# Kernel optimization log

Measured on AMD Instinct MI355X. Metric: run time of the kernel, lower is better.

Reference implementation:

```python
import jax, jax.numpy as jnp
import numpy as np

L = 8192   # residues / nodes
E = 524288 # contact-map edges (avg degree 64)
NEG_SLOPE = 0.2  # PyG GATConv default negative_slope


def gat_layer(x, src, dst, Wg, asrc, adst, bias):
    """PyG-style GATConv (v1), concat heads, eval mode (no dropout).
    x: [L, F_in]; Wg: [F_in, H*C]; asrc/adst: [H, C]; bias: [H*C]."""
    H, C = asrc.shape
    h = (x @ Wg).reshape(L, H, C)                      # [L,H,C]
    a_s = jnp.einsum('nhc,hc->nh', h, asrc)            # [L,H]
    a_d = jnp.einsum('nhc,hc->nh', h, adst)            # [L,H]
    e = jax.nn.leaky_relu(a_s[src] + a_d[dst], NEG_SLOPE)  # [E',H]
    # softmax over incoming edges of each destination node
    m = jax.ops.segment_max(e, dst, num_segments=L)
    ex = jnp.exp(e - m[dst])
    denom = jax.ops.segment_sum(ex, dst, num_segments=L)
    alpha = ex / (denom[dst] + 1e-16)                  # [E',H]
    msg = h[src] * alpha[:, :, None]                   # [E',H,C]
    out = jax.ops.segment_sum(msg, dst, num_segments=L)  # [L,H,C]
    return out.reshape(L, H * C) + bias


def setup_inputs() -> dict:
    key = jax.random.key(0)
    ks = jax.random.split(key, 16)
    def g(k, shape, scale=0.05):
        return (jax.random.normal(k, shape, dtype=jnp.float32) * scale)
    return {
        'input_seq': jax.random.normal(ks[0], (1, L, 26), dtype=jnp.float32),
        'edge_index': jax.random.randint(ks[1], (2, E), 0, L, dtype=jnp.int32),
        'W1': g(ks[2], (26, 1024)),
        'W2': g(ks[3], (1024, 256)),
        'Wg1': g(ks[4], (256, 256)),
        'asrc1': g(ks[5], (4, 64)),
        'adst1': g(ks[6], (4, 64)),
        'b1': g(ks[7], (256,)),
        'Wg2': g(ks[8], (256, 512)),
        'asrc2': g(ks[9], (4, 128)),
        'adst2': g(ks[10], (4, 128)),
        'b2': g(ks[11], (512,)),
        'fcW': g(ks[12], (512, 512)),
        'fcb': g(ks[13], (512,)),
        'outW': g(ks[14], (512, 489)),
        'outb': g(ks[15], (489,)),
    }


def reference(input_seq, edge_index, W1, W2, Wg1, asrc1, adst1, b1,
              Wg2, asrc2, adst2, b2, fcW, fcb, outW, outb):
    # input_layer: Linear(26,1024,no bias) -> ReLU -> Linear(1024,256,no bias)
    x = jax.nn.relu(input_seq[0] @ W1) @ W2            # [L,256]
    # add self-loops (PyG GATConv default)
    loops = jnp.arange(L, dtype=edge_index.dtype)
    src = jnp.concatenate([edge_index[0], loops])
    dst = jnp.concatenate([edge_index[1], loops])
    # two GAT layers with ReLU activation
    x = jax.nn.relu(gat_layer(x, src, dst, Wg1, asrc1, adst1, b1))  # [L,256]
    x = jax.nn.relu(gat_layer(x, src, dst, Wg2, asrc2, adst2, b2))  # [L,512]
    # sum-pool over residues (x.sum(dim=1) with batch=1)
    pooled = x.sum(axis=0, keepdims=True)              # [1,512]
    # fc layers (dropout inactive in eval)
    h = jax.nn.relu(pooled @ fcW + fcb)                # [1,512]
    return h @ outW + outb                             # [1,489]
```

## Files before the change

### kernel.cpp

```cpp
#include <hip/hip_runtime.h>
#include <hip/hip_bf16.h>

constexpr int L = 8192;
constexpr int H = 4;

typedef __attribute__((ext_vector_type(8))) short bf16x8;
typedef __attribute__((ext_vector_type(8))) unsigned short u16x8;
typedef __attribute__((ext_vector_type(4))) float f32x4;

static __device__ __forceinline__ float lrelu(float e) {
  return e > 0.f ? e : 0.2f * e;
}
static __device__ __forceinline__ float b2f(unsigned short s) {
  return __uint_as_float(((unsigned)s) << 16);
}
static __device__ __forceinline__ unsigned short f2b(float f) {
  __hip_bfloat16 h = __float2bfloat16(f);
  return *reinterpret_cast<unsigned short*>(&h);
}

__global__ __launch_bounds__(256) void conv_combo(
    const float* __restrict__ seq, const float* __restrict__ W1,
    const float* __restrict__ W2, const float* __restrict__ Wg1,
    const float* __restrict__ Wg2, const float* __restrict__ fcW,
    const float* __restrict__ outW, const int* __restrict__ ei,
    const float* __restrict__ as1, const float* __restrict__ ad1,
    const float* __restrict__ as2, const float* __restrict__ ad2,
    int E, int Etot,
    __hip_bfloat16* __restrict__ xb, __hip_bfloat16* __restrict__ W1t,
    __hip_bfloat16* __restrict__ W2t, __hip_bfloat16* __restrict__ Wg1t,
    __hip_bfloat16* __restrict__ Wg2t, float* __restrict__ fcWt,
    float* __restrict__ outWt, float* __restrict__ wa2,
    int* __restrict__ deg, int* __restrict__ rank) {
  __shared__ float tile[32][33];
  if (blockIdx.x < 992) {
    int b = blockIdx.x;
    const float* src; void* dst; bool obf16; int K, N, Kout, kt, nt;
    if (b < 256)               { src = W2;  dst = W2t;  obf16 = true;  K = 1024; N = 256; Kout = 1024; nt = b & 7;  kt = b >> 3; }
    else if ((b -= 256) < 64)  { src = Wg1; dst = Wg1t; obf16 = true;  K = 256;  N = 256; Kout = 256;  nt = b & 7;  kt = b >> 3; }
    else if ((b -= 64) < 128)  { src = Wg2; dst = Wg2t; obf16 = true;  K = 256;  N = 512; Kout = 256;  nt = b & 15; kt = b >> 4; }
    else if ((b -= 128) < 256) { src = fcW; dst = fcWt; obf16 = false; K = 512;  N = 512; Kout = 512;  nt = b & 15; kt = b >> 4; }
    else if ((b -= 256) < 256) { src = outW;dst = outWt;obf16 = false; K = 512;  N = 489; Kout = 512;  nt = b & 15; kt = b >> 4; }
    else { b -= 256;             src = W1;  dst = W1t;  obf16 = true;  K = 26;   N = 1024;Kout = 32;   nt = b;      kt = 0; }
    int t = threadIdx.x;
    int lr = t >> 3, lc4 = (t & 7) * 4;
    int gk = kt * 32 + lr, gn = nt * 32 + lc4;
    float4 v = {0.f, 0.f, 0.f, 0.f};
    if (gk < K) {
      const float* p = &src[(size_t)gk * N + gn];
      v.x = (gn + 0 < N) ? p[0] : 0.f;
      v.y = (gn + 1 < N) ? p[1] : 0.f;
      v.z = (gn + 2 < N) ? p[2] : 0.f;
      v.w = (gn + 3 < N) ? p[3] : 0.f;
    }
    tile[lr][lc4 + 0] = v.x; tile[lr][lc4 + 1] = v.y;
    tile[lr][lc4 + 2] = v.z; tile[lr][lc4 + 3] = v.w;
    __syncthreads();
    int on = nt * 32 + lr, ok = kt * 32 + lc4;
    if (on >= N || ok >= Kout) return;
    float o0 = tile[lc4 + 0][lr], o1 = tile[lc4 + 1][lr];
    float o2 = tile[lc4 + 2][lr], o3 = tile[lc4 + 3][lr];
    if (obf16) {
      ushort4 u = {f2b(o0), f2b(o1), f2b(o2), f2b(o3)};
      *(ushort4*)&((__hip_bfloat16*)dst)[(size_t)on * Kout + ok] = u;
    } else {
      float4 u = {o0, o1, o2, o3};
      *(float4*)&((float*)dst)[(size_t)on * Kout + ok] = u;
    }
    return;
  }
  int i = (blockIdx.x - 992) * 256 + threadIdx.x;
  if (i < 262144) { int r = i >> 5, k = i & 31;
    xb[i] = __float2bfloat16(k < 26 ? seq[r * 26 + k] : 0.f); return; }
  i -= 262144;
  if (i < 2048) {
    int k = i >> 3, o = i & 7, h = o & 3;
    const float* av = (o < 4) ? as1 : ad1;
    float s = 0.f;
    for (int c = 0; c < 64; c++) s += Wg1[k * 256 + h * 64 + c] * av[h * 64 + c];
    Wg1t[(size_t)(256 + o) * 256 + k] = __float2bfloat16(s); return; }
  i -= 2048;
  if (i < 2048) {
    int k = i >> 3, o = i & 7, h = o & 3;
    const float* av = (o < 4) ? as2 : ad2;
    float s = 0.f;
    for (int c = 0; c < 128; c++) s += Wg2[k * 512 + h * 128 + c] * av[h * 128 + c];
    wa2[i] = s; return; }
  i -= 2048;
  if (i < 14336) {
    ((__hip_bfloat16*)Wg1t)[(size_t)264 * 256 + i] = __float2bfloat16(0.f); return; }
  i -= 14336;
  if (i < Etot) {
    int dst = (i < E) ? ei[E + i] : (i - E);
    rank[i] = atomicAdd(&deg[dst], 1);
  }
}

template<int BK, bool RELU, bool ASD>
__global__ __launch_bounds__(256) void gemm_big(
    const __hip_bfloat16* __restrict__ A, const __hip_bfloat16* __restrict__ Bt,
    __hip_bfloat16* __restrict__ C, float* __restrict__ asd,
    int M, int N, int K) {
  __shared__ __align__(16) short As[128][BK + 8];
  __shared__ __align__(16) short Bs[64][BK + 8];
  int tid = threadIdx.x;
  int m0 = blockIdx.y * 128, n0 = blockIdx.x * 64;
  int w = tid >> 6, lane = tid & 63;
  int wm = (w >> 1) * 64, wn = (w & 1) * 32;
  f32x4 acc[4][2] = {};
  for (int k0 = 0; k0 < K; k0 += BK) {
    if constexpr (BK == 64) {
#pragma unroll
      for (int i = 0; i < 4; i++) {
        int ch = i * 256 + tid; int r = ch >> 3, kg = ch & 7;
        *(bf16x8*)&As[r][kg * 8] = *(const bf16x8*)&A[(size_t)(m0 + r) * K + k0 + kg * 8];
      }
#pragma unroll
      for (int i = 0; i < 2; i++) {
        int ch = i * 256 + tid; int r = ch >> 3, kg = ch & 7;
        *(bf16x8*)&Bs[r][kg * 8] = *(const bf16x8*)&Bt[(size_t)(n0 + r) * K + k0 + kg * 8];
      }
    } else {
#pragma unroll
      for (int i = 0; i < 2; i++) {
        int ch = i * 256 + tid; int r = ch >> 2, kg = ch & 3;
        *(bf16x8*)&As[r][kg * 8] = *(const bf16x8*)&A[(size_t)(m0 + r) * K + k0 + kg * 8];
      }
      { int r = tid >> 2, kg = tid & 3;
        *(bf16x8*)&Bs[r][kg * 8] = *(const bf16x8*)&Bt[(size_t)(n0 + r) * K + k0 + kg * 8]; }
    }
    __syncthreads();
    int kk = (lane >> 4) * 8;
#pragma unroll
    for (int ks = 0; ks < BK / 32; ks++) {
      bf16x8 af[4], bfr[2];
#pragma unroll
      for (int m = 0; m < 4; m++)
        af[m] = *(const bf16x8*)&As[wm + m * 16 + (lane & 15)][ks * 32 + kk];
#pragma unroll
      for (int n = 0; n < 2; n++)
        bfr[n] = *(const bf16x8*)&Bs[wn + n * 16 + (lane & 15)][ks * 32 + kk];
#pragma unroll
      for (int m = 0; m < 4; m++)
#pragma unroll
        for (int n = 0; n < 2; n++)
          acc[m][n] = __builtin_amdgcn_mfma_f32_16x16x32_bf16(af[m], bfr[n], acc[m][n], 0, 0, 0);
    }
    __syncthreads();
  }
#pragma unroll
  for (int m = 0; m < 4; m++) {
#pragma unroll
    for (int n = 0; n < 2; n++) {
      int col = n0 + wn + n * 16 + (lane & 15);
#pragma unroll
      for (int j = 0; j < 4; j++) {
        int row = m0 + wm + m * 16 + (lane >> 4) * 4 + j;
        float v = acc[m][n][j];
        if (RELU) v = fmaxf(v, 0.f);
        if (!ASD) {
          C[(size_t)row * N + col] = __float2bfloat16(v);
        } else {
          if (col < N) C[(size_t)row * N + col] = __float2bfloat16(v);
          else if (col < N + 8) asd[(size_t)row * 8 + (col - N)] = v;
        }
      }
    }
  }
}

__global__ __launch_bounds__(1024) void scan_deg(const int* __restrict__ deg,
                                                 int* __restrict__ row_start,
                                                 float* __restrict__ pooled) {
  __shared__ int wsum[16];
  int t = threadIdx.x;
  if (t < 512) pooled[t] = 0.f;
  int lane = t & 63, w = t >> 6;
  int local[8];
  int sum = 0;
#pragma unroll
  for (int j = 0; j < 8; j++) { local[j] = deg[t * 8 + j]; sum += local[j]; }
  int v = sum;
#pragma unroll
  for (int off = 1; off < 64; off <<= 1) {
    int u = __shfl_up(v, off);
    if (lane >= off) v += u;
  }
  if (lane == 63) wsum[w] = v;
  __syncthreads();
  int woff = 0;
  for (int i = 0; i < w; i++) woff += wsum[i];
  int base = woff + v - sum;
#pragma unroll
  for (int j = 0; j < 8; j++) { row_start[t * 8 + j] = base; base += local[j]; }
  if (t == 1023) row_start[L] = base;
}

__global__ void scatter_edges(const int* __restrict__ ei, int E, int Etot,
                              const int* __restrict__ row_start,
                              const int* __restrict__ rank, int* __restrict__ csr_src) {
  int e = blockIdx.x * blockDim.x + threadIdx.x;
  if (e >= Etot) return;
  int srcv, dstv;
  if (e < E) { srcv = ei[e]; dstv = ei[E + e]; } else { srcv = dstv = e - E; }
  csr_src[row_start[dstv] + rank[e]] = srcv;
}

template<int C, int PHASES, bool ASD2>
__global__ __launch_bounds__(128) void gat_fused(
    const __hip_bfloat16* __restrict__ hfeat, const float* __restrict__ a_sd,
    const int* __restrict__ row_start, const int* __restrict__ csr_src,
    const float* __restrict__ bias, __hip_bfloat16* __restrict__ out,
    const float* __restrict__ wa2, float* __restrict__ a_sd2) {
  constexpr int HC = 4 * C;
  constexpr int CP = HC / PHASES;
  constexpr int BATCH = 16;
  static_assert(CP == 256, "phase width must be 256");
  int wid = threadIdx.x >> 6, lane = threadIdx.x & 63;
  int n = blockIdx.x * 2 + wid;
  int c0 = blockIdx.y * CP + lane * 4;
  int hh = c0 / C;
  int rs = row_start[n], re = row_start[n + 1];
  float4 ad4 = *(const float4*)&a_sd[(size_t)n * 8 + 4];
  float bv[4];
#pragma unroll
  for (int k = 0; k < 4; k++) bv[k] = bias[c0 + k];

  __shared__ float s_w[2][64][4];
  float dp[4] = {0.f, 0.f, 0.f, 0.f};
  float acc[4] = {0.f, 0.f, 0.f, 0.f};
  const unsigned short* hbase = (const unsigned short*)hfeat;

  int base = rs;
  int cnt = min(64, re - rs);
  int srcv = 0;
  float4 as4 = {0.f, 0.f, 0.f, 0.f};
  if (lane < cnt) {
    srcv = csr_src[rs + lane];
    as4 = *(const float4*)&a_sd[(size_t)srcv * 8];
  }

  while (base < re) {
    float w0 = 0.f, w1 = 0.f, w2 = 0.f, w3 = 0.f;
    if (lane < cnt) {
      w0 = __expf(lrelu(as4.x + ad4.x));
      w1 = __expf(lrelu(as4.y + ad4.y));
      w2 = __expf(lrelu(as4.z + ad4.z));
      w3 = __expf(lrelu(as4.w + ad4.w));
    }
    dp[0] += w0; dp[1] += w1; dp[2] += w2; dp[3] += w3;
    float4 wv = {w0, w1, w2, w3};
    *(float4*)&s_w[wid][lane][0] = wv;
    asm volatile("s_waitcnt lgkmcnt(0)" ::: "memory");
    int cur_src = srcv;
    int cur_cnt = cnt;
    int nbase = base + 64;
    bool have_next = nbase < re;
    cnt = min(64, re - nbase);
    srcv = 0;
    if (have_next && lane < cnt) srcv = csr_src[nbase + lane];
    float4 nas4 = {0.f, 0.f, 0.f, 0.f};
    bool did_asd = false;

    int j = 0;
    for (; j + BATCH <= cur_cnt; j += BATCH) {
      int srs[BATCH];
#pragma unroll
      for (int k = 0; k < BATCH; k++) srs[k] = __builtin_amdgcn_readlane(cur_src, j + k);
      ushort4 v[BATCH];
#pragma unroll
      for (int k = 0; k < BATCH; k++)
        v[k] = *(const ushort4*)&hbase[(size_t)srs[k] * HC + c0];
      if (j == BATCH && have_next) {
        if (lane < cnt) nas4 = *(const float4*)&a_sd[(size_t)srcv * 8];
        did_asd = true;
      }
#pragma unroll
      for (int k = 0; k < BATCH; k++) {
        float av = s_w[wid][j + k][hh];
        acc[0] = fmaf(av, b2f(v[k].x), acc[0]);
        acc[1] = fmaf(av, b2f(v[k].y), acc[1]);
        acc[2] = fmaf(av, b2f(v[k].z), acc[2]);
        acc[3] = fmaf(av, b2f(v[k].w), acc[3]);
      }
    }
    if (have_next && !did_asd && lane < cnt)
      nas4 = *(const float4*)&a_sd[(size_t)srcv * 8];
    for (; j < cur_cnt; j++) {
      int sr = __builtin_amdgcn_readlane(cur_src, j);
      float av = s_w[wid][j][hh];
      ushort4 v = *(const ushort4*)&hbase[(size_t)sr * HC + c0];
      acc[0] = fmaf(av, b2f(v.x), acc[0]);
      acc[1] = fmaf(av, b2f(v.y), acc[1]);
      acc[2] = fmaf(av, b2f(v.z), acc[2]);
      acc[3] = fmaf(av, b2f(v.w), acc[3]);
    }
    as4 = nas4;
    base = nbase;
  }

#pragma unroll
  for (int off = 32; off > 0; off >>= 1) {
#pragma unroll
    for (int h = 0; h < 4; h++) dp[h] += __shfl_xor(dp[h], off);
  }
  float dsel = hh == 0 ? dp[0] : hh == 1 ? dp[1] : hh == 2 ? dp[2] : dp[3];
  float inv = 1.f / (dsel + 1e-16f);

#pragma unroll
  for (int k = 0; k < 4; k++)
    acc[k] = fmaxf(fmaf(acc[k], inv, bv[k]), 0.f);
  ushort4 ov = {f2b(acc[0]), f2b(acc[1]), f2b(acc[2]), f2b(acc[3])};
  *(ushort4*)((unsigned short*)out + (size_t)n * HC + c0) = ov;

  if constexpr (ASD2) {
    float p[8] = {};
#pragma unroll
    for (int q = 0; q < 4; q++) {
      const float* wr = &wa2[(size_t)(c0 + q) * 8];
#pragma unroll
      for (int o = 0; o < 8; o++) p[o] = fmaf(acc[q], wr[o], p[o]);
    }
#pragma unroll
    for (int off = 32; off > 0; off >>= 1) {
#pragma unroll
      for (int o = 0; o < 8; o++) p[o] += __shfl_xor(p[o], off);
    }
    if (lane == 0) {
      float4 p0 = {p[0], p[1], p[2], p[3]};
      float4 p1 = {p[4], p[5], p[6], p[7]};
      *(float4*)&a_sd2[(size_t)n * 8 + 0] = p0;
      *(float4*)&a_sd2[(size_t)n * 8 + 4] = p1;
    }
  }
}

__global__ __launch_bounds__(512) void col_sum_bf16(const __hip_bfloat16* __restrict__ x,
                                                    float* __restrict__ pooled) {
  int t = threadIdx.x;
  float acc = 0.f;
  for (int r = blockIdx.x; r < L; r += 64)
    acc += b2f(*(const unsigned short*)&x[(size_t)r * 512 + t]);
  atomicAdd(&pooled[t], acc);
}

__global__ __launch_bounds__(256) void fc1(const float* __restrict__ pooled,
                                           const float* __restrict__ Wt,
                                           const float* __restrict__ b,
                                           float* __restrict__ out) {
  __shared__ float pv[512];
  __shared__ float red[256];
  int t = threadIdx.x;
  pv[t] = pooled[t]; pv[t + 256] = pooled[t + 256];
  __syncthreads();
  int ol = t >> 4;
  int o = blockIdx.x * 16 + ol;
  int ks = (t & 15) * 32;
  float p = 0.f;
  const float* wr = &Wt[(size_t)o * 512 + ks];
#pragma unroll
  for (int kk = 0; kk < 32; kk++) p = fmaf(pv[ks + kk], wr[kk], p);
  red[t] = p;
  __syncthreads();
  if ((t & 15) == 0) {
    float s2 = 0.f;
#pragma unroll
    for (int i = 0; i < 16; i++) s2 += red[ol * 16 + i];
    out[o] = fmaxf(s2 + b[o], 0.f);
  }
}

__global__ __launch_bounds__(256) void fc2(const float* __restrict__ h,
                                           const float* __restrict__ Wt,
                                           const float* __restrict__ outb,
                                           float* __restrict__ out) {
  __shared__ float pv[512];
  __shared__ float red[256];
  int t = threadIdx.x;
  pv[t] = h[t]; pv[t + 256] = h[t + 256];
  __syncthreads();
  int ol = t >> 4;
  int o = blockIdx.x * 16 + ol;
  int ks = (t & 15) * 32;
  float p = 0.f;
  const float* wr = &Wt[(size_t)o * 512 + ks];
#pragma unroll
  for (int kk = 0; kk < 32; kk++) p = fmaf(pv[ks + kk], wr[kk], p);
  red[t] = p;
  __syncthreads();
  if ((t & 15) == 0 && o < 489) {
    float s2 = 0.f;
#pragma unroll
    for (int i = 0; i < 16; i++) s2 += red[ol * 16 + i];
    out[o] = s2 + outb[o];
  }
}

extern "C" void kernel_launch(void* const* d_in, const int* in_sizes, int n_in,
                              void* d_out, int out_size, void* d_ws, size_t ws_size,
                              hipStream_t stream) {
  const float* seq   = (const float*)d_in[0];
  const int*   ei    = (const int*)d_in[1];
  const float* W1    = (const float*)d_in[2];
  const float* W2    = (const float*)d_in[3];
  const float* Wg1   = (const float*)d_in[4];
  const float* asrc1 = (const float*)d_in[5];
  const float* adst1 = (const float*)d_in[6];
  const float* b1    = (const float*)d_in[7];
  const float* Wg2   = (const float*)d_in[8];
  const float* asrc2 = (const float*)d_in[9];
  const float* adst2 = (const float*)d_in[10];
  const float* b2    = (const float*)d_in[11];
  const float* fcW   = (const float*)d_in[12];
  const float* fcb   = (const float*)d_in[13];
  const float* outW  = (const float*)d_in[14];
  const float* outb  = (const float*)d_in[15];
  float* outp = (float*)d_out;

  const int E = in_sizes[1] / 2;
  const int Etot = E + L;

  char* ws = (char*)d_ws;
  __hip_bfloat16* mlp1 = (__hip_bfloat16*)(ws + 0);
  __hip_bfloat16* out2 = (__hip_bfloat16*)(ws + 0);
  __hip_bfloat16* h2   = (__hip_bfloat16*)(ws + (16u << 20));
  __hip_bfloat16* x0   = (__hip_bfloat16*)(ws + (24u << 20));
  __hip_bfloat16* h1   = (__hip_bfloat16*)(ws + (28u << 20));
  __hip_bfloat16* out1 = (__hip_bfloat16*)(ws + (32u << 20));
  size_t off = (36u << 20);
  __hip_bfloat16* xb   = (__hip_bfloat16*)(ws + off); off += (size_t)L * 32 * 2;
  __hip_bfloat16* W1t  = (__hip_bfloat16*)(ws + off); off += (size_t)1024 * 32 * 2;
  __hip_bfloat16* W2t  = (__hip_bfloat16*)(ws + off); off += (size_t)256 * 1024 * 2;
  __hip_bfloat16* Wg1t = (__hip_bfloat16*)(ws + off); off += (size_t)320 * 256 * 2;
  __hip_bfloat16* Wg2t = (__hip_bfloat16*)(ws + off); off += (size_t)512 * 256 * 2;
  float* fcWt  = (float*)(ws + off); off += (size_t)512 * 512 * 4;
  float* outWt = (float*)(ws + off); off += (size_t)512 * 512 * 4;
  int* csr_src = (int*)(ws + off); off += (size_t)Etot * 4;
  int* rank    = (int*)(ws + off); off += (size_t)Etot * 4;
  off = (off + 255) & ~(size_t)255;
  int* row_start = (int*)(ws + off); off += (size_t)(L + 1) * 4;
  off = (off + 255) & ~(size_t)255;
  int* deg    = (int*)(ws + off); off += (size_t)L * 4;
  float* a_sd1 = (float*)(ws + off); off += (size_t)L * 8 * 4;
  float* a_sd2 = (float*)(ws + off); off += (size_t)L * 8 * 4;
  float* wa2 = (float*)(ws + off); off += 2048 * 4;
  float* pooled = (float*)(ws + off); off += 512 * 4;
  float* hbuf   = (float*)(ws + off); off += 512 * 4;

  hipMemsetAsync(deg, 0, (size_t)L * 4, stream);

  int convN = 262144 + 2048 + 2048 + 14336 + Etot;
  int convB = (convN + 255) / 256;
  conv_combo<<<992 + convB, 256, 0, stream>>>(
      seq, W1, W2, Wg1, Wg2, fcW, outW, ei, asrc1, adst1, asrc2, adst2, E, Etot,
      xb, W1t, W2t, Wg1t, Wg2t, fcWt, outWt, wa2, deg, rank);

  scan_deg<<<1, 1024, 0, stream>>>(deg, row_start, pooled);
  scatter_edges<<<(Etot + 255) / 256, 256, 0, stream>>>(ei, E, Etot, row_start, rank, csr_src);

  gemm_big<32, true, false><<<dim3(16, 64), 256, 0, stream>>>(xb, W1t, mlp1, nullptr, L, 1024, 32);
  gemm_big<64, false, false><<<dim3(4, 64), 256, 0, stream>>>(mlp1, W2t, x0, nullptr, L, 256, 1024);

  gemm_big<64, false, true><<<dim3(5, 64), 256, 0, stream>>>(x0, Wg1t, h1, a_sd1, L, 256, 256);
  gat_fused<64, 1, true><<<dim3(4096, 1), 128, 0, stream>>>(h1, a_sd1, row_start, csr_src, b1, out1, wa2, a_sd2);

  gemm_big<64, false, false><<<dim3(8, 64), 256, 0, stream>>>(out1, Wg2t, h2, nullptr, L, 512, 256);
  gat_fused<128, 2, false><<<dim3(4096, 2), 128, 0, stream>>>(h2, a_sd2, row_start, csr_src, b2, out2, nullptr, nullptr);

  col_sum_bf16<<<64, 512, 0, stream>>>(out2, pooled);
  fc1<<<32, 256, 0, stream>>>(pooled, fcWt, fcb, hbuf);
  fc2<<<31, 256, 0, stream>>>(hbuf, outWt, outb, outp);
}
```

Baseline: 221.7 us.

## Precompute GAT attention weights and softmax denominators in a separate kernel

Adds a calc_alpha kernel that computes the per-edge exp(leaky_relu) attention weights once, stores them as bf16 along with per-node inverse denominators, and then has gat_fused read these instead of recomputing them. The aim is to stop the second GAT layer's two column-phase blocks from each redoing the exp, gather and reduction work, and to drop the dependent a_sd gather from the aggregation loop. In exchange it adds two kernel launches, an extra read/write pass over edge-sized alpha data, and rounds the unnormalised weights to bf16, which loses some precision.

```diff
diff --git a/kernel.cpp b/kernel.cpp
--- a/kernel.cpp
+++ b/kernel.cpp
@@ -206,9 +206,42 @@
   csr_src[row_start[dstv] + rank[e]] = srcv;
 }
 
+__global__ __launch_bounds__(256) void calc_alpha(
+    const float* __restrict__ a_sd, const int* __restrict__ row_start,
+    const int* __restrict__ csr_src, unsigned short* __restrict__ alpha,
+    float* __restrict__ inv4) {
+  int wid = threadIdx.x >> 6, lane = threadIdx.x & 63;
+  int n = blockIdx.x * 4 + wid;
+  int rs = row_start[n], re = row_start[n + 1];
+  float4 ad4 = *(const float4*)&a_sd[(size_t)n * 8 + 4];
+  float dp[4] = {0.f, 0.f, 0.f, 0.f};
+  for (int base = rs + lane; base < re; base += 64) {
+    int src = csr_src[base];
+    float4 as4 = *(const float4*)&a_sd[(size_t)src * 8];
+    float w0 = __expf(lrelu(as4.x + ad4.x));
+    float w1 = __expf(lrelu(as4.y + ad4.y));
+    float w2 = __expf(lrelu(as4.z + ad4.z));
+    float w3 = __expf(lrelu(as4.w + ad4.w));
+    dp[0] += w0; dp[1] += w1; dp[2] += w2; dp[3] += w3;
+    ushort4 wv = {f2b(w0), f2b(w1), f2b(w2), f2b(w3)};
+    *(ushort4*)&alpha[(size_t)base * 4] = wv;
+  }
+#pragma unroll
+  for (int off = 32; off > 0; off >>= 1) {
+#pragma unroll
+    for (int h = 0; h < 4; h++) dp[h] += __shfl_xor(dp[h], off);
+  }
+  if (lane == 0) {
+    float4 iv = {1.f / (dp[0] + 1e-16f), 1.f / (dp[1] + 1e-16f),
+                 1.f / (dp[2] + 1e-16f), 1.f / (dp[3] + 1e-16f)};
+    *(float4*)&inv4[(size_t)n * 4] = iv;
+  }
+}
+
 template<int C, int PHASES, bool ASD2>
 __global__ __launch_bounds__(128) void gat_fused(
-    const __hip_bfloat16* __restrict__ hfeat, const float* __restrict__ a_sd,
+    const __hip_bfloat16* __restrict__ hfeat,
+    const unsigned short* __restrict__ alpha, const float* __restrict__ inv4,
     const int* __restrict__ row_start, const int* __restrict__ csr_src,
     const float* __restrict__ bias, __hip_bfloat16* __restrict__ out,
     const float* __restrict__ wa2, float* __restrict__ a_sd2) {
@@ -221,35 +254,26 @@
   int c0 = blockIdx.y * CP + lane * 4;
   int hh = c0 / C;
   int rs = row_start[n], re = row_start[n + 1];
-  float4 ad4 = *(const float4*)&a_sd[(size_t)n * 8 + 4];
+  float4 iv4 = *(const float4*)&inv4[(size_t)n * 4];
   float bv[4];
 #pragma unroll
   for (int k = 0; k < 4; k++) bv[k] = bias[c0 + k];
 
   __shared__ float s_w[2][64][4];
-  float dp[4] = {0.f, 0.f, 0.f, 0.f};
   float acc[4] = {0.f, 0.f, 0.f, 0.f};
   const unsigned short* hbase = (const unsigned short*)hfeat;
 
   int base = rs;
   int cnt = min(64, re - rs);
   int srcv = 0;
-  float4 as4 = {0.f, 0.f, 0.f, 0.f};
+  ushort4 av4 = {0, 0, 0, 0};
   if (lane < cnt) {
     srcv = csr_src[rs + lane];
-    as4 = *(const float4*)&a_sd[(size_t)srcv * 8];
+    av4 = *(const ushort4*)&alpha[(size_t)(rs + lane) * 4];
   }
 
   while (base < re) {
-    float w0 = 0.f, w1 = 0.f, w2 = 0.f, w3 = 0.f;
-    if (lane < cnt) {
-      w0 = __expf(lrelu(as4.x + ad4.x));
-      w1 = __expf(lrelu(as4.y + ad4.y));
-      w2 = __expf(lrelu(as4.z + ad4.z));
-      w3 = __expf(lrelu(as4.w + ad4.w));
-    }
-    dp[0] += w0; dp[1] += w1; dp[2] += w2; dp[3] += w3;
-    float4 wv = {w0, w1, w2, w3};
+    float4 wv = {b2f(av4.x), b2f(av4.y), b2f(av4.z), b2f(av4.w)};
     *(float4*)&s_w[wid][lane][0] = wv;
     asm volatile("s_waitcnt lgkmcnt(0)" ::: "memory");
     int cur_src = srcv;
@@ -258,9 +282,11 @@
     bool have_next = nbase < re;
     cnt = min(64, re - nbase);
     srcv = 0;
-    if (have_next && lane < cnt) srcv = csr_src[nbase + lane];
-    float4 nas4 = {0.f, 0.f, 0.f, 0.f};
-    bool did_asd = false;
+    ushort4 nav4 = {0, 0, 0, 0};
+    if (have_next && lane < cnt) {
+      srcv = csr_src[nbase + lane];
+      nav4 = *(const ushort4*)&alpha[(size_t)(nbase + lane) * 4];
+    }
 
     int j = 0;
     for (; j + BATCH <= cur_cnt; j += BATCH) {
@@ -271,10 +297,6 @@
 #pragma unroll
       for (int k = 0; k < BATCH; k++)
         v[k] = *(const ushort4*)&hbase[(size_t)srs[k] * HC + c0];
-      if (j == BATCH && have_next) {
-        if (lane < cnt) nas4 = *(const float4*)&a_sd[(size_t)srcv * 8];
-        did_asd = true;
-      }
 #pragma unroll
       for (int k = 0; k < BATCH; k++) {
         float av = s_w[wid][j + k][hh];
@@ -284,8 +306,6 @@
         acc[3] = fmaf(av, b2f(v[k].w), acc[3]);
       }
     }
-    if (have_next && !did_asd && lane < cnt)
-      nas4 = *(const float4*)&a_sd[(size_t)srcv * 8];
     for (; j < cur_cnt; j++) {
       int sr = __builtin_amdgcn_readlane(cur_src, j);
       float av = s_w[wid][j][hh];
@@ -295,17 +315,11 @@
       acc[2] = fmaf(av, b2f(v.z), acc[2]);
       acc[3] = fmaf(av, b2f(v.w), acc[3]);
     }
-    as4 = nas4;
+    av4 = nav4;
     base = nbase;
   }
 
-#pragma unroll
-  for (int off = 32; off > 0; off >>= 1) {
-#pragma unroll
-    for (int h = 0; h < 4; h++) dp[h] += __shfl_xor(dp[h], off);
-  }
-  float dsel = hh == 0 ? dp[0] : hh == 1 ? dp[1] : hh == 2 ? dp[2] : dp[3];
-  float inv = 1.f / (dsel + 1e-16f);
+  float inv = hh == 0 ? iv4.x : hh == 1 ? iv4.y : hh == 2 ? iv4.z : iv4.w;
 
 #pragma unroll
   for (int k = 0; k < 4; k++)
@@ -423,6 +437,7 @@
   char* ws = (char*)d_ws;
   __hip_bfloat16* mlp1 = (__hip_bfloat16*)(ws + 0);
   __hip_bfloat16* out2 = (__hip_bfloat16*)(ws + 0);
+  unsigned short* alpha = (unsigned short*)(ws + (8u << 20));
   __hip_bfloat16* h2   = (__hip_bfloat16*)(ws + (16u << 20));
   __hip_bfloat16* x0   = (__hip_bfloat16*)(ws + (24u << 20));
   __hip_bfloat16* h1   = (__hip_bfloat16*)(ws + (28u << 20));
@@ -443,6 +458,8 @@
   int* deg    = (int*)(ws + off); off += (size_t)L * 4;
   float* a_sd1 = (float*)(ws + off); off += (size_t)L * 8 * 4;
   float* a_sd2 = (float*)(ws + off); off += (size_t)L * 8 * 4;
+  float* inv1 = (float*)(ws + off); off += (size_t)L * 4 * 4;
+  float* inv2 = (float*)(ws + off); off += (size_t)L * 4 * 4;
   float* wa2 = (float*)(ws + off); off += 2048 * 4;
   float* pooled = (float*)(ws + off); off += 512 * 4;
   float* hbuf   = (float*)(ws + off); off += 512 * 4;
@@ -462,10 +479,12 @@
   gemm_big<64, false, false><<<dim3(4, 64), 256, 0, stream>>>(mlp1, W2t, x0, nullptr, L, 256, 1024);
 
   gemm_big<64, false, true><<<dim3(5, 64), 256, 0, stream>>>(x0, Wg1t, h1, a_sd1, L, 256, 256);
-  gat_fused<64, 1, true><<<dim3(4096, 1), 128, 0, stream>>>(h1, a_sd1, row_start, csr_src, b1, out1, wa2, a_sd2);
+  calc_alpha<<<2048, 256, 0, stream>>>(a_sd1, row_start, csr_src, alpha, inv1);
+  gat_fused<64, 1, true><<<dim3(4096, 1), 128, 0, stream>>>(h1, alpha, inv1, row_start, csr_src, b1, out1, wa2, a_sd2);
 
   gemm_big<64, false, false><<<dim3(8, 64), 256, 0, stream>>>(out1, Wg2t, h2, nullptr, L, 512, 256);
-  gat_fused<128, 2, false><<<dim3(4096, 2), 128, 0, stream>>>(h2, a_sd2, row_start, csr_src, b2, out2, nullptr, nullptr);
+  calc_alpha<<<2048, 256, 0, stream>>>(a_sd2, row_start, csr_src, alpha, inv2);
+  gat_fused<128, 2, false><<<dim3(4096, 2), 128, 0, stream>>>(h2, alpha, inv2, row_start, csr_src, b2, out2, nullptr, nullptr);
 
   col_sum_bf16<<<64, 512, 0, stream>>>(out2, pooled);
   fc1<<<32, 256, 0, stream>>>(pooled, fcWt, fcb, hbuf);
```

After: 232.1 us. +4.7%, slower.

## Cover full GAT row per wave with bf16 dot2 edge accumulation

Applied to the files above, without the earlier changes.

The second GAT layer previously used two column phases, each a separate block that walked the same edge list and recomputed the softmax weights. Now one wave covers all 512 channels with 8-wide bf16 loads, which halves edge-list traversal and exp work. The softmax weights are stored in LDS as bf16 with masks for each half, so a packed bf16 dot2 instruction does two multiply-adds per instruction. The inner batch is cut to 8 to limit register growth. Rounding the attention weights to bf16 lowers precision, and the fallback path without dot2 only reads the low-half weight.

```diff
diff --git a/kernel.cpp b/kernel.cpp
--- a/kernel.cpp
+++ b/kernel.cpp
@@ -8,6 +8,18 @@
 typedef __attribute__((ext_vector_type(8))) unsigned short u16x8;
 typedef __attribute__((ext_vector_type(4))) float f32x4;
 
+#if defined(__has_builtin)
+#  if __has_builtin(__builtin_amdgcn_fdot2_f32_bf16)
+#    define HAVE_DOT2 1
+#  endif
+#endif
+#ifndef HAVE_DOT2
+#  define HAVE_DOT2 0
+#endif
+#if HAVE_DOT2
+typedef __attribute__((ext_vector_type(2))) __bf16 bfx2;
+#endif
+
 static __device__ __forceinline__ float lrelu(float e) {
   return e > 0.f ? e : 0.2f * e;
 }
@@ -17,6 +29,26 @@
 static __device__ __forceinline__ unsigned short f2b(float f) {
   __hip_bfloat16 h = __float2bfloat16(f);
   return *reinterpret_cast<unsigned short*>(&h);
+}
+
+template<int PAIRS>
+static __device__ __forceinline__ void edge_fma(const unsigned* hv, uint2 m, float* acc) {
+#if HAVE_DOT2
+#pragma unroll
+  for (int p = 0; p < PAIRS; p++) {
+    acc[2 * p]     = __builtin_amdgcn_fdot2_f32_bf16(
+        __builtin_bit_cast(bfx2, hv[p]), __builtin_bit_cast(bfx2, m.x), acc[2 * p], false);
+    acc[2 * p + 1] = __builtin_amdgcn_fdot2_f32_bf16(
+        __builtin_bit_cast(bfx2, hv[p]), __builtin_bit_cast(bfx2, m.y), acc[2 * p + 1], false);
+  }
+#else
+  float af = b2f((unsigned short)(m.x & 0xffffu));
+#pragma unroll
+  for (int p = 0; p < PAIRS; p++) {
+    acc[2 * p]     = fmaf(af, b2f((unsigned short)(hv[p] & 0xffffu)), acc[2 * p]);
+    acc[2 * p + 1] = fmaf(af, b2f((unsigned short)(hv[p] >> 16)), acc[2 * p + 1]);
+  }
+#endif
 }
 
 __global__ __launch_bounds__(256) void conv_combo(
@@ -206,29 +238,26 @@
   csr_src[row_start[dstv] + rank[e]] = srcv;
 }
 
-template<int C, int PHASES, bool ASD2>
+template<int C, bool ASD2>
 __global__ __launch_bounds__(128) void gat_fused(
     const __hip_bfloat16* __restrict__ hfeat, const float* __restrict__ a_sd,
     const int* __restrict__ row_start, const int* __restrict__ csr_src,
     const float* __restrict__ bias, __hip_bfloat16* __restrict__ out,
     const float* __restrict__ wa2, float* __restrict__ a_sd2) {
   constexpr int HC = 4 * C;
-  constexpr int CP = HC / PHASES;
-  constexpr int BATCH = 16;
-  static_assert(CP == 256, "phase width must be 256");
+  constexpr int VEC = HC / 64;
+  constexpr int PAIRS = VEC / 2;
+  constexpr int BATCH = 8;
   int wid = threadIdx.x >> 6, lane = threadIdx.x & 63;
   int n = blockIdx.x * 2 + wid;
-  int c0 = blockIdx.y * CP + lane * 4;
-  int hh = c0 / C;
+  int c0 = lane * VEC;
+  int hh = lane >> 4;
   int rs = row_start[n], re = row_start[n + 1];
   float4 ad4 = *(const float4*)&a_sd[(size_t)n * 8 + 4];
-  float bv[4];
-#pragma unroll
-  for (int k = 0; k < 4; k++) bv[k] = bias[c0 + k];
-
-  __shared__ float s_w[2][64][4];
+
+  __shared__ __align__(16) uint2 s_m[2][64][4];
   float dp[4] = {0.f, 0.f, 0.f, 0.f};
-  float acc[4] = {0.f, 0.f, 0.f, 0.f};
+  float acc[VEC] = {};
   const unsigned short* hbase = (const unsigned short*)hfeat;
 
   int base = rs;
@@ -249,8 +278,11 @@
       w3 = __expf(lrelu(as4.w + ad4.w));
     }
     dp[0] += w0; dp[1] += w1; dp[2] += w2; dp[3] += w3;
-    float4 wv = {w0, w1, w2, w3};
-    *(float4*)&s_w[wid][lane][0] = wv;
+    unsigned l0 = f2b(w0), l1 = f2b(w1), l2 = f2b(w2), l3 = f2b(w3);
+    uint4 ma = {l0, l0 << 16, l1, l1 << 16};
+    uint4 mb = {l2, l2 << 16, l3, l3 << 16};
+    *(uint4*)&s_m[wid][lane][0] = ma;
+    *(uint4*)&s_m[wid][lane][2] = mb;
     asm volatile("s_waitcnt lgkmcnt(0)" ::: "memory");
     int cur_src = srcv;
     int cur_cnt = cnt;
@@ -267,33 +299,33 @@
       int srs[BATCH];
 #pragma unroll
       for (int k = 0; k < BATCH; k++) srs[k] = __builtin_amdgcn_readlane(cur_src, j + k);
-      ushort4 v[BATCH];
-#pragma unroll
-      for (int k = 0; k < BATCH; k++)
-        v[k] = *(const ushort4*)&hbase[(size_t)srs[k] * HC + c0];
-      if (j == BATCH && have_next) {
+      unsigned hv[BATCH][PAIRS];
+#pragma unroll
+      for (int k = 0; k < BATCH; k++) {
+        const unsigned short* hp = &hbase[(size_t)srs[k] * HC + c0];
+        if constexpr (PAIRS == 4) *(uint4*)&hv[k][0] = *(const uint4*)hp;
+        else                      *(uint2*)&hv[k][0] = *(const uint2*)hp;
+      }
+      if (j == 0 && have_next) {
         if (lane < cnt) nas4 = *(const float4*)&a_sd[(size_t)srcv * 8];
         did_asd = true;
       }
 #pragma unroll
       for (int k = 0; k < BATCH; k++) {
-        float av = s_w[wid][j + k][hh];
-        acc[0] = fmaf(av, b2f(v[k].x), acc[0]);
-        acc[1] = fmaf(av, b2f(v[k].y), acc[1]);
-        acc[2] = fmaf(av, b2f(v[k].z), acc[2]);
-        acc[3] = fmaf(av, b2f(v[k].w), acc[3]);
+        uint2 m = s_m[wid][j + k][hh];
+        edge_fma<PAIRS>(hv[k], m, acc);
       }
     }
     if (have_next && !did_asd && lane < cnt)
       nas4 = *(const float4*)&a_sd[(size_t)srcv * 8];
     for (; j < cur_cnt; j++) {
       int sr = __builtin_amdgcn_readlane(cur_src, j);
-      float av = s_w[wid][j][hh];
-      ushort4 v = *(const ushort4*)&hbase[(size_t)sr * HC + c0];
-      acc[0] = fmaf(av, b2f(v.x), acc[0]);
-      acc[1] = fmaf(av, b2f(v.y), acc[1]);
-      acc[2] = fmaf(av, b2f(v.z), acc[2]);
-      acc[3] = fmaf(av, b2f(v.w), acc[3]);
+      unsigned hv[PAIRS];
+      const unsigned short* hp = &hbase[(size_t)sr * HC + c0];
+      if constexpr (PAIRS == 4) *(uint4*)&hv[0] = *(const uint4*)hp;
+      else                      *(uint2*)&hv[0] = *(const uint2*)hp;
+      uint2 m = s_m[wid][j][hh];
+      edge_fma<PAIRS>(hv, m, acc);
     }
     as4 = nas4;
     base = nbase;
@@ -308,15 +340,23 @@
   float inv = 1.f / (dsel + 1e-16f);
 
 #pragma unroll
-  for (int k = 0; k < 4; k++)
-    acc[k] = fmaxf(fmaf(acc[k], inv, bv[k]), 0.f);
-  ushort4 ov = {f2b(acc[0]), f2b(acc[1]), f2b(acc[2]), f2b(acc[3])};
-  *(ushort4*)((unsigned short*)out + (size_t)n * HC + c0) = ov;
+  for (int k = 0; k < VEC; k++)
+    acc[k] = fmaxf(fmaf(acc[k], inv, bias[c0 + k]), 0.f);
+  unsigned short* op = (unsigned short*)out + (size_t)n * HC + c0;
+  if constexpr (VEC == 8) {
+    u16x8 ov;
+#pragma unroll
+    for (int k = 0; k < 8; k++) ov[k] = f2b(acc[k]);
+    *(u16x8*)op = ov;
+  } else {
+    ushort4 ov = {f2b(acc[0]), f2b(acc[1]), f2b(acc[2]), f2b(acc[3])};
+    *(ushort4*)op = ov;
+  }
 
   if constexpr (ASD2) {
     float p[8] = {};
 #pragma unroll
-    for (int q = 0; q < 4; q++) {
+    for (int q = 0; q < VEC; q++) {
       const float* wr = &wa2[(size_t)(c0 + q) * 8];
 #pragma unroll
       for (int o = 0; o < 8; o++) p[o] = fmaf(acc[q], wr[o], p[o]);
@@ -462,10 +502,10 @@
   gemm_big<64, false, false><<<dim3(4, 64), 256, 0, stream>>>(mlp1, W2t, x0, nullptr, L, 256, 1024);
 
   gemm_big<64, false, true><<<dim3(5, 64), 256, 0, stream>>>(x0, Wg1t, h1, a_sd1, L, 256, 256);
-  gat_fused<64, 1, true><<<dim3(4096, 1), 128, 0, stream>>>(h1, a_sd1, row_start, csr_src, b1, out1, wa2, a_sd2);
+  gat_fused<64, true><<<4096, 128, 0, stream>>>(h1, a_sd1, row_start, csr_src, b1, out1, wa2, a_sd2);
 
   gemm_big<64, false, false><<<dim3(8, 64), 256, 0, stream>>>(out1, Wg2t, h2, nullptr, L, 512, 256);
-  gat_fused<128, 2, false><<<dim3(4096, 2), 128, 0, stream>>>(h2, a_sd2, row_start, csr_src, b2, out2, nullptr, nullptr);
+  gat_fused<128, false><<<4096, 128, 0, stream>>>(h2, a_sd2, row_start, csr_src, b2, out2, nullptr, nullptr);
 
   col_sum_bf16<<<64, 512, 0, stream>>>(out2, pooled);
   fc1<<<32, 256, 0, stream>>>(pooled, fcWt, fcb, hbuf);
```

Measured after the change: 221.7 us. No clear change (+0.0%).
